# Kernel optimization log

Hardware: AMD Instinct MI355X
Metric: run time of the kernel (lower is better)

The kernel has to match this reference:

```python
import jax, jax.numpy as jnp
import numpy as np

B, L, C = 8, 2048, 256
D = C // 8  # qk head dim = 32


def _attn(q, k, v, scale):
    # q:[B,L,D] k:[B,L,D] v:[B,L,Dv] -> [B,L,Dv]
    scores = jnp.einsum('bld,bmd->blm', q, k) / scale
    w = jax.nn.softmax(scores, axis=-1)
    return jnp.einsum('blm,bmd->bld', w, v)


def setup_inputs() -> dict:
    key = jax.random.key(0)
    ks = jax.random.split(key, 16)
    he = lambda k, cin, cout: jax.random.normal(k, (cin, cout), jnp.float32) * np.sqrt(2.0 / cin)
    inp = {'x': jax.random.normal(ks[0], (B, L, C, 2), jnp.float32)}
    # 12 1x1 conv kernels (no bias): Q/K -> C//8, V -> C, for 4 attention blocks
    dims = [D, D, C, D, D, C, D, D, C, D, D, C]
    for i, dout in enumerate(dims):
        inp[f'w{i+1}'] = he(ks[i + 1], C, dout)
    inp['alpha'] = jnp.zeros((1,), jnp.float32)
    inp['gamma'] = jnp.zeros((1,), jnp.float32)
    return inp


def reference(x, w1, w2, w3, w4, w5, w6, w7, w8, w9, w10, w11, w12, alpha, gamma):
    ecg = x[:, :, :, 0]  # [B,L,C]
    pcg = x[:, :, :, 1]
    proj = lambda f, w: jnp.einsum('blc,cd->bld', f, w)  # 1x1 conv, no bias
    scale = jnp.sqrt(jnp.asarray(D, x.dtype))

    # ECG intra-attention
    qkv_ecg_intra = _attn(proj(ecg, w1), proj(ecg, w2), proj(ecg, w3), scale)
    # ECG inter-attention (Q from ECG, K/V from PCG)
    qkv_ecg_inter = _attn(proj(ecg, w4), proj(pcg, w5), proj(pcg, w6), scale)
    ecg_out = qkv_ecg_inter + alpha * qkv_ecg_intra

    # PCG intra-attention
    qkv_pcg_intra = _attn(proj(pcg, w7), proj(pcg, w8), proj(pcg, w9), scale)
    # PCG inter-attention (Q from PCG, K/V from ECG)
    qkv_pcg_inter = _attn(proj(pcg, w10), proj(ecg, w11), proj(ecg, w12), scale)
    pcg_out = qkv_pcg_inter + gamma * qkv_pcg_intra

    return jnp.concatenate([ecg_out, pcg_out], axis=-1)  # [B,L,2C]
```

## Files before the change

### kernel.cpp

```cpp
#include <hip/hip_runtime.h>


typedef __bf16 v8bf __attribute__((ext_vector_type(8)));
typedef float  v16f __attribute__((ext_vector_type(16)));
typedef unsigned int u32;

typedef __attribute__((address_space(1))) const void gvoid;
typedef __attribute__((address_space(3))) void svoid;

#define QSCALE 0.25500526817276613f

union frag_u { u32 d[4]; v8bf v; };
union pk_u { unsigned short s[2]; u32 d; };

static __device__ inline u32 pack_bf16(float x, float y) {
  pk_u u;
  __bf16 a = (__bf16)x, b = (__bf16)y;
  u.s[0] = *(unsigned short*)&a;
  u.s[1] = *(unsigned short*)&b;
  return u.d;
}

__global__ __launch_bounds__(256) void deint_kernel(const float* __restrict__ x,
                                                    __bf16* __restrict__ xe,
                                                    __bf16* __restrict__ xp) {
  const size_t i = (size_t)blockIdx.x * 256 + threadIdx.x;
  const float4* xin = (const float4*)(x + i * 16);
  float4 a = xin[0], b = xin[1], c = xin[2], d = xin[3];
  v8bf ev, pv;
  ev[0]=(__bf16)a.x; ev[1]=(__bf16)a.z; ev[2]=(__bf16)b.x; ev[3]=(__bf16)b.z;
  ev[4]=(__bf16)c.x; ev[5]=(__bf16)c.z; ev[6]=(__bf16)d.x; ev[7]=(__bf16)d.z;
  pv[0]=(__bf16)a.y; pv[1]=(__bf16)a.w; pv[2]=(__bf16)b.y; pv[3]=(__bf16)b.w;
  pv[4]=(__bf16)c.y; pv[5]=(__bf16)c.w; pv[6]=(__bf16)d.y; pv[7]=(__bf16)d.w;
  *(v8bf*)(xe + i * 8) = ev;
  *(v8bf*)(xp + i * 8) = pv;
}

struct ProjArgs {
  const __bf16* xe;
  const __bf16* xp;
  const float* w[12];
  __bf16* q[4];
  __bf16* k[4];
  __bf16* vt[4];
  const float* alpha;
  const float* gamma;
};

__global__ __launch_bounds__(256) void proj_kernel(ProjArgs pa) {
  const int job = blockIdx.x;
  const int rb  = blockIdx.y * 128;
  const int tid = threadIdx.x;
  const int lane = tid & 63, w = tid >> 6;
  const int l31 = lane & 31, lh = lane >> 5;
  const int l7 = lane & 7, l8 = lane >> 3;

  if (job >= 4) {
    const int vi = (job - 4) >> 2;
    if (vi == 0 && pa.alpha[0] == 0.0f) return;
    if (vi == 3 && pa.gamma[0] == 0.0f) return;
  }

  __shared__ __bf16 lds_b[64][264];
  __shared__ __bf16 lds_a[2][128 * 64];

  int src, dout, wc0[2], vcol0 = 0, vmode = 0;
  const float* wp[2];
  __bf16* dqk[2] = {nullptr, nullptr};
  __bf16* vdst = nullptr;
  float sc = 1.0f;
  if (job < 4) {
    dout = 32; wc0[0] = 0; wc0[1] = 0;
    switch (job) {
      case 0: src=0; wp[0]=pa.w[0]; wp[1]=pa.w[3];  dqk[0]=pa.q[0]; dqk[1]=pa.q[1]; sc=QSCALE; break;
      case 1: src=0; wp[0]=pa.w[1]; wp[1]=pa.w[10]; dqk[0]=pa.k[0]; dqk[1]=pa.k[3]; break;
      case 2: src=1; wp[0]=pa.w[6]; wp[1]=pa.w[9];  dqk[0]=pa.q[2]; dqk[1]=pa.q[3]; sc=QSCALE; break;
      default:src=1; wp[0]=pa.w[4]; wp[1]=pa.w[7];  dqk[0]=pa.k[1]; dqk[1]=pa.k[2]; break;
    }
  } else {
    const int vi = (job - 4) >> 2, t = (job - 4) & 3;
    const int widx = (vi==0) ? 2 : (vi==1) ? 11 : (vi==2) ? 5 : 8;
    const int vbuf = (vi==0) ? 0 : (vi==1) ? 3  : (vi==2) ? 1 : 2;
    dout = 256; vmode = 1; src = vi >> 1;
    wp[0] = pa.w[widx]; wp[1] = pa.w[widx];
    wc0[0] = t*64; wc0[1] = t*64 + 32;
    vcol0 = t*64; vdst = pa.vt[vbuf];
  }

  for (int h = 0; h < 2; ++h) {
    const float* wgt = wp[h]; const int c0 = wc0[h];
    for (int i = tid; i < 32*256; i += 256) {
      int n = i & 31, kk = i >> 5;
      lds_b[h*32 + n][kk] = (__bf16)wgt[(size_t)kk*dout + c0 + n];
    }
  }

  const __bf16* X = src ? pa.xp : pa.xe;
  const char* agbase = (const char*)(X + (size_t)rb*256) + (size_t)(l7 ^ l8)*16
                     + (size_t)l8*512;

#define STAGE_A(buf, kb)                                                        \
  {                                                                             \
    const char* g = agbase + (size_t)(kb)*128;                                  \
    _Pragma("unroll")                                                           \
    for (int i = 0; i < 4; ++i)                                                 \
      __builtin_amdgcn_global_load_lds(                                         \
          (gvoid*)(g + (size_t)(w*4 + i)*8*512),                                \
          (svoid*)&lds_a[buf][((w*4 + i)*8)*64 + lane*8], 16, 0, 0);            \
  }

  STAGE_A(0, 0)
  __syncthreads();

  v16f acc[2];
#pragma unroll
  for (int n = 0; n < 2; ++n)
#pragma unroll
    for (int i = 0; i < 16; ++i) acc[n][i] = 0.f;

  for (int kb = 0; kb < 4; ++kb) {
    if (kb < 3) STAGE_A((kb + 1) & 1, kb + 1)
    const __bf16* ab = &lds_a[kb & 1][0];
#pragma unroll
    for (int kk = 0; kk < 4; ++kk) {
      const v8bf af = *(const v8bf*)&ab[(w*32 + l31)*64 + (((kk*2 + lh) ^ (l31 & 7))*8)];
#pragma unroll
      for (int nt = 0; nt < 2; ++nt) {
        const v8bf bf = *(const v8bf*)&lds_b[nt*32 + l31][kb*64 + kk*16 + lh*8];
        acc[nt] = __builtin_amdgcn_mfma_f32_32x32x16_bf16(af, bf, acc[nt], 0, 0, 0);
      }
    }
    __syncthreads();
  }

  if (!vmode) {
#pragma unroll
    for (int nt = 0; nt < 2; ++nt) {
      __bf16* dst = dqk[nt];
#pragma unroll
      for (int r = 0; r < 16; ++r) {
        const int row = rb + w*32 + (r & 3) + 8*(r >> 2) + 4*lh;
        dst[(size_t)row*32 + l31] = (__bf16)(acc[nt][r] * sc);
      }
    }
  } else {
    __bf16 (*lds_t)[136] = (__bf16 (*)[136])&lds_a[0][0];
#pragma unroll
    for (int nt = 0; nt < 2; ++nt) {
#pragma unroll
      for (int r = 0; r < 16; ++r) {
        const int row = w*32 + (r & 3) + 8*(r >> 2) + 4*lh;
        lds_t[nt*32 + l31][row] = (__bf16)acc[nt][r];
      }
    }
    __syncthreads();
    const int bb = rb >> 11, ll0 = rb & 2047;
    const int nt0 = vcol0 >> 5;
    const size_t tbase = (size_t)(bb*32 + (ll0 >> 6));
    for (int i = tid; i < 1024; i += 256) {
      const int ktl = i >> 9, s = i & 511;
      const int h = s >> 8, kc2 = (s >> 5) & 7, v5 = s & 31;
      const int vrow = h*32 + v5, krow = ktl*64 + kc2*8;
      *(int4*)&vdst[((tbase + ktl)*2048 + (size_t)((nt0 + h)*8 + kc2)*32 + v5) * 8] =
          *(const int4*)&lds_t[vrow][krow];
    }
  }
}

struct FlashArgs {
  const __bf16* q[4];
  const __bf16* k[4];
  const __bf16* v[4];
  const float* alpha;
  const float* gamma;
  float* out;
};

template<int NTN>
__device__ __forceinline__ void flash_body(
    const __bf16* __restrict__ Qp, const __bf16* __restrict__ Kb,
    const char* __restrict__ vgbase, float scv, float* __restrict__ outp,
    __bf16* __restrict__ lds0, int lane, int w, int l31, int lh) {

  __bf16* vb0 = lds0;
  __bf16* vb1 = lds0 + NTN*2048;

  const v8bf qf0 = *(const v8bf*)&Qp[lh*8];
  const v8bf qf1 = *(const v8bf*)&Qp[16 + lh*8];

#define STAGE_V(dst_, kt_)                                                      \
  {                                                                             \
    const char* g = vgbase + (size_t)(kt_)*32768;                               \
    _Pragma("unroll")                                                           \
    for (int i = 0; i < NTN; ++i)                                               \
      __builtin_amdgcn_global_load_lds(                                         \
          (gvoid*)(g + (size_t)i*1024),                                         \
          (svoid*)&dst_[(w*NTN*64 + 64*i)*8 + lane*8], 16, 0, 0);               \
  }

  v16f acc[NTN];
#pragma unroll
  for (int n = 0; n < NTN; ++n)
#pragma unroll
    for (int i = 0; i < 16; ++i) acc[n][i] = 0.f;

  float den_s = 0.f;
  v8bf pf[4];
  v8bf kf00, kf01, kf10, kf11;
  v16f st0, st1;
  u32 pk0[8], pk1[8];

#define LOADK(kt_)                                                              \
  {                                                                             \
    const int kb_ = (kt_) * 64;                                                 \
    kf00 = *(const v8bf*)&Kb[((size_t)(kb_ +      l31))*32 +      lh*8];        \
    kf01 = *(const v8bf*)&Kb[((size_t)(kb_ +      l31))*32 + 16 + lh*8];        \
    kf10 = *(const v8bf*)&Kb[((size_t)(kb_ + 32 + l31))*32 +      lh*8];        \
    kf11 = *(const v8bf*)&Kb[((size_t)(kb_ + 32 + l31))*32 + 16 + lh*8];        \
  }

#define SMFMA                                                                   \
  {                                                                             \
    _Pragma("unroll")                                                           \
    for (int i = 0; i < 16; ++i) { st0[i] = 0.f; st1[i] = 0.f; }                \
    st0 = __builtin_amdgcn_mfma_f32_32x32x16_bf16(kf00, qf0, st0, 0, 0, 0);     \
    st0 = __builtin_amdgcn_mfma_f32_32x32x16_bf16(kf01, qf1, st0, 0, 0, 0);     \
    st1 = __builtin_amdgcn_mfma_f32_32x32x16_bf16(kf10, qf0, st1, 0, 0, 0);     \
    st1 = __builtin_amdgcn_mfma_f32_32x32x16_bf16(kf11, qf1, st1, 0, 0, 0);     \
  }

#define EXPH(st_, pk_)                                                          \
  _Pragma("unroll")                                                             \
  for (int i = 0; i < 8; ++i) {                                                 \
    const float e0 = __builtin_exp2f(st_[2*i]);                                 \
    const float e1 = __builtin_exp2f(st_[2*i + 1]);                             \
    den_s += e0 + e1;                                                           \
    pk_[i] = pack_bf16(e0, e1);                                                 \
  }

#define XCHG(pk_, o_)                                                           \
  _Pragma("unroll")                                                             \
  for (int f2 = 0; f2 < 2; ++f2) {                                              \
    u32 a0 = pk_[f2*4 + 0], b0 = pk_[f2*4 + 2];                                 \
    u32 a1 = pk_[f2*4 + 1], b1 = pk_[f2*4 + 3];                                 \
    asm("v_permlane32_swap_b32 %0, %1" : "+v"(a0), "+v"(b0));                   \
    asm("v_permlane32_swap_b32 %0, %1" : "+v"(a1), "+v"(b1));                   \
    frag_u fu;                                                                  \
    fu.d[0] = a0; fu.d[1] = a1; fu.d[2] = b0; fu.d[3] = b1;                     \
    pf[(o_) + f2] = fu.v;                                                       \
  }

#define PVBLK(kc_, vb_)                                                         \
  _Pragma("unroll")                                                             \
  for (int nt = 0; nt < NTN; ++nt) {                                            \
    const v8bf vf = *(const v8bf*)&vb_[(nt*256 + (kc_)*64 + lane)*8];           \
    acc[nt] = __builtin_amdgcn_mfma_f32_32x32x16_bf16(pf[kc_], vf, acc[nt], 0, 0, 0); \
  }

  LOADK(0)
  STAGE_V(vb0, 0)
  SMFMA
  EXPH(st0, pk0)
  EXPH(st1, pk1)
  XCHG(pk0, 0)
  XCHG(pk1, 2)
  __syncthreads();

  for (int kt = 0; kt < 31; ++kt) {
    const int cur = kt & 1;
    LOADK(kt + 1)
    if (cur) { STAGE_V(vb0, kt + 1) } else { STAGE_V(vb1, kt + 1) }
    const __bf16* vb = cur ? vb1 : vb0;

    PVBLK(0, vb)
    SMFMA
    PVBLK(1, vb)
    EXPH(st0, pk0)
    PVBLK(2, vb)
    EXPH(st1, pk1)
    XCHG(pk0, 0)
    PVBLK(3, vb)
    XCHG(pk1, 2)

    __syncthreads();
  }

  {
    PVBLK(0, vb1)
    PVBLK(1, vb1)
    PVBLK(2, vb1)
    PVBLK(3, vb1)
  }

  const float den_full = den_s + __shfl_xor(den_s, 32, 64);
#pragma unroll
  for (int r = 0; r < 16; ++r) {
    const int row = (r & 3) + 8*(r >> 2) + 4*lh;
    const float f = scv / __shfl(den_full, row, 64);
#pragma unroll
    for (int nt = 0; nt < NTN; ++nt)
      unsafeAtomicAdd(&outp[(size_t)row*512 + nt*32 + l31], acc[nt][r] * f);
  }

#undef STAGE_V
#undef LOADK
#undef SMFMA
#undef EXPH
#undef XCHG
#undef PVBLK
}

__global__ __launch_bounds__(256, 2) void flash_kernel(FlashArgs fa) {
  const int flat = blockIdx.x;
  const int pair = flat & 31, qt = flat >> 5;
  const int att = pair & 3, bb = pair >> 2;
  const int tid = threadIdx.x;
  const int lane = tid & 63, w = tid >> 6;
  const int l31 = lane & 31, lh = lane >> 5;

  __shared__ __bf16 v_lds[2][16384];

  const float av = fa.alpha[0], gv = fa.gamma[0];
  float scv = 1.0f;
  int att_e = att, nt0 = 0;
  bool half = false;
  if (att == 0)      { if (av == 0.0f) { att_e = 1; nt0 = 4; half = true; } else scv = av; }
  else if (att == 1) { half = (av == 0.0f); }
  else if (att == 2) { if (gv == 0.0f) { att_e = 3; nt0 = 4; half = true; } else scv = gv; }
  else               { half = (gv == 0.0f); }

  const __bf16* Qp = fa.q[att_e] + (size_t)(bb*2048 + qt*128 + w*32 + l31)*32;
  const __bf16* Kb = fa.k[att_e] + (size_t)bb*2048*32;
  const char* Vb   = (const char*)(fa.v[att_e] + (size_t)bb*32*16384);
  float* outp = fa.out + (size_t)(bb*2048 + qt*128 + w*32)*512
              + (att_e >> 1)*256 + nt0*32;

  if (half) {
    const char* vgbase = Vb + (size_t)(nt0*256 + w*256 + lane)*16;
    flash_body<4>(Qp, Kb, vgbase, scv, outp, &v_lds[0][0], lane, w, l31, lh);
  } else {
    const char* vgbase = Vb + (size_t)(w*512 + lane)*16;
    flash_body<8>(Qp, Kb, vgbase, scv, outp, &v_lds[0][0], lane, w, l31, lh);
  }
}

extern "C" void kernel_launch(void* const* d_in, const int* in_sizes, int n_in,
                              void* d_out, int out_size, void* d_ws, size_t ws_size,
                              hipStream_t stream) {
  (void)in_sizes; (void)n_in; (void)out_size; (void)ws_size;

  __bf16* wsp = (__bf16*)d_ws;
  const size_t XE = (size_t)16384 * 256;
  const size_t QK = (size_t)16384 * 32;
  const size_t VT = (size_t)8 * 32 * 16384;

  __bf16* xe = wsp;
  __bf16* xp = wsp + XE;

  ProjArgs pa;
  pa.xe = xe; pa.xp = xp;
  const float* x = (const float*)d_in[0];
  for (int i = 0; i < 12; ++i) pa.w[i] = (const float*)d_in[1 + i];
  __bf16* base = wsp + 2*XE;
  for (int i = 0; i < 4; ++i) pa.q[i]  = base + (size_t)i * QK;
  for (int i = 0; i < 4; ++i) pa.k[i]  = base + (size_t)(4 + i) * QK;
  for (int i = 0; i < 4; ++i) pa.vt[i] = base + 8*QK + (size_t)i * VT;
  pa.alpha = (const float*)d_in[13];
  pa.gamma = (const float*)d_in[14];

  hipMemsetAsync(d_out, 0, (size_t)8*2048*512*4, stream);
  hipLaunchKernelGGL(deint_kernel, dim3(2048), dim3(256), 0, stream, x, xe, xp);
  hipLaunchKernelGGL(proj_kernel, dim3(20, 128), dim3(256), 0, stream, pa);

  FlashArgs fl;
  for (int i = 0; i < 4; ++i) { fl.q[i] = pa.q[i]; fl.k[i] = pa.k[i]; fl.v[i] = pa.vt[i]; }
  fl.alpha = (const float*)d_in[13];
  fl.gamma = (const float*)d_in[14];
  fl.out = (float*)d_out;
  hipLaunchKernelGGL(flash_kernel, dim3(512), dim3(256), 0, stream, fl);
}
```

Baseline: 229.0 us.

## Split flash attention into dedicated half-width and full-width kernels

The attention kernel is split in two. A specialized half-width kernel handles the case where alpha/gamma are zero: it uses a smaller LDS buffer, targets 3 blocks per CU, and writes output with plain stores instead of atomics. A separate full kernel handles the nonzero-coefficient case, and each kernel exits early for blocks that do not apply. This lowers register and LDS pressure on the common path, at the cost of an extra kernel launch whose blocks mostly return immediately.

```diff
diff --git a/kernel.cpp b/kernel.cpp
--- a/kernel.cpp
+++ b/kernel.cpp
@@ -176,6 +176,146 @@
   float* out;
 };
 
+__global__ __launch_bounds__(256, 3) void flash_half(FlashArgs fa) {
+  const int flat = blockIdx.x;
+  const int pair = flat & 31, qt = flat >> 5;
+  const int att = pair & 3, bb = pair >> 2;
+  const int tid = threadIdx.x;
+  const int lane = tid & 63, w = tid >> 6;
+  const int l31 = lane & 31, lh = lane >> 5;
+
+  const float av = fa.alpha[0], gv = fa.gamma[0];
+  int att_e, nt0;
+  if (att == 0)      { if (av != 0.0f) return; att_e = 1; nt0 = 4; }
+  else if (att == 1) { if (av != 0.0f) return; att_e = 1; nt0 = 0; }
+  else if (att == 2) { if (gv != 0.0f) return; att_e = 3; nt0 = 4; }
+  else               { if (gv != 0.0f) return; att_e = 3; nt0 = 0; }
+
+  __shared__ __bf16 v_lds[2][8192];
+
+  const __bf16* Qp = fa.q[att_e] + (size_t)(bb*2048 + qt*128 + w*32 + l31)*32;
+  const __bf16* Kb = fa.k[att_e] + (size_t)bb*2048*32;
+  const char* vgbase = (const char*)(fa.v[att_e] + (size_t)bb*32*16384)
+                     + (size_t)(nt0*256 + w*256 + lane)*16;
+  float* outp = fa.out + (size_t)(bb*2048 + qt*128 + w*32)*512
+              + (att_e >> 1)*256 + nt0*32;
+
+  const v8bf qf0 = *(const v8bf*)&Qp[lh*8];
+  const v8bf qf1 = *(const v8bf*)&Qp[16 + lh*8];
+
+#define HSTAGE(buf_, kt_)                                                       \
+  {                                                                             \
+    const char* g = vgbase + (size_t)(kt_)*32768;                               \
+    _Pragma("unroll")                                                           \
+    for (int i = 0; i < 4; ++i)                                                 \
+      __builtin_amdgcn_global_load_lds(                                         \
+          (gvoid*)(g + (size_t)i*1024),                                         \
+          (svoid*)&v_lds[buf_][(w*256 + 64*i)*8 + lane*8], 16, 0, 0);           \
+  }
+
+#define HLOADK(a_, b_, c_, d_, kt_)                                             \
+  {                                                                             \
+    const int kb_ = (kt_) * 64;                                                 \
+    a_ = *(const v8bf*)&Kb[((size_t)(kb_ +      l31))*32 +      lh*8];          \
+    b_ = *(const v8bf*)&Kb[((size_t)(kb_ +      l31))*32 + 16 + lh*8];          \
+    c_ = *(const v8bf*)&Kb[((size_t)(kb_ + 32 + l31))*32 +      lh*8];          \
+    d_ = *(const v8bf*)&Kb[((size_t)(kb_ + 32 + l31))*32 + 16 + lh*8];          \
+  }
+
+  v16f acc[4];
+#pragma unroll
+  for (int n = 0; n < 4; ++n)
+#pragma unroll
+    for (int i = 0; i < 16; ++i) acc[n][i] = 0.f;
+  float den_s = 0.f;
+
+  v8bf kfc00, kfc01, kfc10, kfc11;
+  HLOADK(kfc00, kfc01, kfc10, kfc11, 0)
+  HSTAGE(0, 0)
+  __syncthreads();
+
+#pragma unroll 1
+  for (int kt = 0; kt < 32; ++kt) {
+    const int cur = kt & 1;
+    v8bf kfn00, kfn01, kfn10, kfn11;
+    if (kt < 31) {
+      HLOADK(kfn00, kfn01, kfn10, kfn11, kt + 1)
+      HSTAGE(cur ^ 1, kt + 1)
+    }
+
+    v16f st0, st1;
+#pragma unroll
+    for (int i = 0; i < 16; ++i) { st0[i] = 0.f; st1[i] = 0.f; }
+    st0 = __builtin_amdgcn_mfma_f32_32x32x16_bf16(kfc00, qf0, st0, 0, 0, 0);
+    st0 = __builtin_amdgcn_mfma_f32_32x32x16_bf16(kfc01, qf1, st0, 0, 0, 0);
+    st1 = __builtin_amdgcn_mfma_f32_32x32x16_bf16(kfc10, qf0, st1, 0, 0, 0);
+    st1 = __builtin_amdgcn_mfma_f32_32x32x16_bf16(kfc11, qf1, st1, 0, 0, 0);
+
+    u32 pk0[8], pk1[8];
+#pragma unroll
+    for (int i = 0; i < 8; ++i) {
+      const float e0 = __builtin_exp2f(st0[2*i]);
+      const float e1 = __builtin_exp2f(st0[2*i + 1]);
+      den_s += e0 + e1;
+      pk0[i] = pack_bf16(e0, e1);
+    }
+#pragma unroll
+    for (int i = 0; i < 8; ++i) {
+      const float e0 = __builtin_exp2f(st1[2*i]);
+      const float e1 = __builtin_exp2f(st1[2*i + 1]);
+      den_s += e0 + e1;
+      pk1[i] = pack_bf16(e0, e1);
+    }
+
+    v8bf pf[4];
+#pragma unroll
+    for (int f2 = 0; f2 < 2; ++f2) {
+      u32 a0 = pk0[f2*4 + 0], b0 = pk0[f2*4 + 2];
+      u32 a1 = pk0[f2*4 + 1], b1 = pk0[f2*4 + 3];
+      asm("v_permlane32_swap_b32 %0, %1" : "+v"(a0), "+v"(b0));
+      asm("v_permlane32_swap_b32 %0, %1" : "+v"(a1), "+v"(b1));
+      frag_u fu;
+      fu.d[0] = a0; fu.d[1] = a1; fu.d[2] = b0; fu.d[3] = b1;
+      pf[f2] = fu.v;
+    }
+#pragma unroll
+    for (int f2 = 0; f2 < 2; ++f2) {
+      u32 a0 = pk1[f2*4 + 0], b0 = pk1[f2*4 + 2];
+      u32 a1 = pk1[f2*4 + 1], b1 = pk1[f2*4 + 3];
+      asm("v_permlane32_swap_b32 %0, %1" : "+v"(a0), "+v"(b0));
+      asm("v_permlane32_swap_b32 %0, %1" : "+v"(a1), "+v"(b1));
+      frag_u fu;
+      fu.d[0] = a0; fu.d[1] = a1; fu.d[2] = b0; fu.d[3] = b1;
+      pf[2 + f2] = fu.v;
+    }
+
+    const __bf16* vb = &v_lds[cur][0];
+#pragma unroll
+    for (int kc = 0; kc < 4; ++kc)
+#pragma unroll
+      for (int nt = 0; nt < 4; ++nt) {
+        const v8bf vf = *(const v8bf*)&vb[(nt*256 + kc*64 + lane)*8];
+        acc[nt] = __builtin_amdgcn_mfma_f32_32x32x16_bf16(pf[kc], vf, acc[nt], 0, 0, 0);
+      }
+
+    __syncthreads();
+    if (kt < 31) { kfc00 = kfn00; kfc01 = kfn01; kfc10 = kfn10; kfc11 = kfn11; }
+  }
+
+  const float den_full = den_s + __shfl_xor(den_s, 32, 64);
+#pragma unroll
+  for (int r = 0; r < 16; ++r) {
+    const int row = (r & 3) + 8*(r >> 2) + 4*lh;
+    const float f = 1.0f / __shfl(den_full, row, 64);
+#pragma unroll
+    for (int nt = 0; nt < 4; ++nt)
+      outp[(size_t)row*512 + nt*32 + l31] = acc[nt][r] * f;
+  }
+
+#undef HSTAGE
+#undef HLOADK
+}
+
 template<int NTN>
 __device__ __forceinline__ void flash_body(
     const __bf16* __restrict__ Qp, const __bf16* __restrict__ Kb,
@@ -310,7 +450,7 @@
 #undef PVBLK
 }
 
-__global__ __launch_bounds__(256, 2) void flash_kernel(FlashArgs fa) {
+__global__ __launch_bounds__(256, 2) void flash_full(FlashArgs fa) {
   const int flat = blockIdx.x;
   const int pair = flat & 31, qt = flat >> 5;
   const int att = pair & 3, bb = pair >> 2;
@@ -318,30 +458,22 @@
   const int lane = tid & 63, w = tid >> 6;
   const int l31 = lane & 31, lh = lane >> 5;
 
-  __shared__ __bf16 v_lds[2][16384];
-
   const float av = fa.alpha[0], gv = fa.gamma[0];
   float scv = 1.0f;
-  int att_e = att, nt0 = 0;
-  bool half = false;
-  if (att == 0)      { if (av == 0.0f) { att_e = 1; nt0 = 4; half = true; } else scv = av; }
-  else if (att == 1) { half = (av == 0.0f); }
-  else if (att == 2) { if (gv == 0.0f) { att_e = 3; nt0 = 4; half = true; } else scv = gv; }
-  else               { half = (gv == 0.0f); }
-
-  const __bf16* Qp = fa.q[att_e] + (size_t)(bb*2048 + qt*128 + w*32 + l31)*32;
-  const __bf16* Kb = fa.k[att_e] + (size_t)bb*2048*32;
-  const char* Vb   = (const char*)(fa.v[att_e] + (size_t)bb*32*16384);
-  float* outp = fa.out + (size_t)(bb*2048 + qt*128 + w*32)*512
-              + (att_e >> 1)*256 + nt0*32;
-
-  if (half) {
-    const char* vgbase = Vb + (size_t)(nt0*256 + w*256 + lane)*16;
-    flash_body<4>(Qp, Kb, vgbase, scv, outp, &v_lds[0][0], lane, w, l31, lh);
-  } else {
-    const char* vgbase = Vb + (size_t)(w*512 + lane)*16;
-    flash_body<8>(Qp, Kb, vgbase, scv, outp, &v_lds[0][0], lane, w, l31, lh);
-  }
+  if (att == 0)      { if (av == 0.0f) return; scv = av; }
+  else if (att == 1) { if (av == 0.0f) return; }
+  else if (att == 2) { if (gv == 0.0f) return; scv = gv; }
+  else               { if (gv == 0.0f) return; }
+
+  __shared__ __bf16 v_lds[2][16384];
+
+  const __bf16* Qp = fa.q[att] + (size_t)(bb*2048 + qt*128 + w*32 + l31)*32;
+  const __bf16* Kb = fa.k[att] + (size_t)bb*2048*32;
+  const char* vgbase = (const char*)(fa.v[att] + (size_t)bb*32*16384)
+                     + (size_t)(w*512 + lane)*16;
+  float* outp = fa.out + (size_t)(bb*2048 + qt*128 + w*32)*512 + (att >> 1)*256;
+
+  flash_body<8>(Qp, Kb, vgbase, scv, outp, &v_lds[0][0], lane, w, l31, lh);
 }
 
 extern "C" void kernel_launch(void* const* d_in, const int* in_sizes, int n_in,
@@ -377,5 +509,6 @@
   fl.alpha = (const float*)d_in[13];
   fl.gamma = (const float*)d_in[14];
   fl.out = (float*)d_out;
-  hipLaunchKernelGGL(flash_kernel, dim3(512), dim3(256), 0, stream, fl);
-}
+  hipLaunchKernelGGL(flash_half, dim3(512), dim3(256), 0, stream, fl);
+  hipLaunchKernelGGL(flash_full, dim3(512), dim3(256), 0, stream, fl);
+}
```

New measurement: 230.8 us. Within noise of the previous version (+0.8%).
